# Kernel tuning notes

Hardware: AMD Instinct MI355X
Metric: run time of the kernel (lower is better)

## Reference

```python
import jax, jax.numpy as jnp
import numpy as np

BLOCK = 32
# MXFP4 grid: exp_bits=2, man_bits=1, exp_bias=1 -> {0, 0.5, 1, 1.5, 2, 3, 4, 6}
GRID = jnp.array([0.0, 0.5, 1.0, 1.5, 2.0, 3.0, 4.0, 6.0], dtype=jnp.float32)
GRID_MAX = 6.0
EPS = 1e-12


def _snap_to_grid(a):
    # nearest-neighbor snap; ties go to the lower grid value (matches torch ref)
    pos = jnp.searchsorted(GRID, a)              # side='left', same as torch default
    lo = jnp.clip(pos - 1, 0, GRID.shape[0] - 1)
    hi = jnp.clip(pos, 0, GRID.shape[0] - 1)
    v_lo = GRID[lo]
    v_hi = GRID[hi]
    return jnp.where(a - v_lo > v_hi - a, v_hi, v_lo)


def quant_act_mxfp4(x):
    orig_shape = x.shape
    xb = x.astype(jnp.float32).reshape(-1, BLOCK)           # [nblk, BLOCK]
    amax = jnp.clip(jnp.max(jnp.abs(xb), axis=-1, keepdims=True), EPS)
    # scale stored in FP16 (quant_act_fp hard-codes scale_dtype='FP16')
    scale = (amax / GRID_MAX).astype(jnp.float16).astype(jnp.float32)
    x_norm = xb / jnp.clip(scale, EPS)
    snapped = _snap_to_grid(jnp.abs(x_norm))
    return (jnp.sign(x_norm) * snapped * scale).reshape(orig_shape)


def setup_inputs() -> dict:
    key = jax.random.key(0)
    k1, k2, k3 = jax.random.split(key, 3)
    x = jax.random.normal(k1, (2, 4096, 4096), dtype=jnp.float32)
    W = jax.random.normal(k2, (11008, 4096), dtype=jnp.float32)
    bias = jax.random.normal(k3, (11008,), dtype=jnp.float32)
    return {"x": x, "W": W, "bias": bias}


def reference(x, W, bias):
    # 1) dynamic per-block MXFP4 activation quantization
    x_q = quant_act_mxfp4(x)                                # [B, S, H]
    # 2) dense GEMM: F.linear(x_q, W, bias)
    return jnp.einsum('bsh,oh->bso', x_q, W) + bias
```

## Files before the change

### kernel.cpp

```cpp
#include <hip/hip_runtime.h>


#define M_DIM 8192
#define K_DIM 4096
#define N_DIM 11008

typedef float floatx4 __attribute__((ext_vector_type(4)));
typedef _Float16 half8 __attribute__((ext_vector_type(8)));


__device__ inline float snap_mxfp4(float a) {
    float lo  = (a <= 0.25f) ? 0.0f : ((a <= 0.75f) ? 0.5f : 1.0f);
    float mid = (a <= 1.75f) ? 1.5f : 2.0f;
    float hi  = (a <= 3.5f)  ? 3.0f : ((a <= 5.0f) ? 4.0f : 6.0f);
    return (a <= 1.25f) ? lo : ((a <= 2.5f) ? mid : hi);
}

#define QUANT_BLOCKS 16384
#define CONV_BLOCKS  22016

__global__ __launch_bounds__(256) void prep_kernel(
        const float* __restrict__ x, _Float16* __restrict__ xq,
        const float* __restrict__ W, _Float16* __restrict__ wq) {
    if (blockIdx.x < QUANT_BLOCKS) {
        size_t t    = (size_t)blockIdx.x * 256 + threadIdx.x;
        size_t base = t * 8;
        const float4* p = (const float4*)(x + base);
        float4 v0 = p[0];
        float4 v1 = p[1];
        float in[8] = {v0.x, v0.y, v0.z, v0.w, v1.x, v1.y, v1.z, v1.w};

        float a0 = fmaxf(fmaxf(fabsf(in[0]), fabsf(in[1])), fmaxf(fabsf(in[2]), fabsf(in[3])));
        float a1 = fmaxf(fmaxf(fabsf(in[4]), fabsf(in[5])), fmaxf(fabsf(in[6]), fabsf(in[7])));
        float amax = fmaxf(a0, a1);
        amax = fmaxf(amax, __shfl_xor(amax, 1));
        amax = fmaxf(amax, __shfl_xor(amax, 2));
        amax = fmaxf(amax, 1e-12f);

        float scale = (float)(_Float16)(amax / 6.0f);
        float sdiv  = fmaxf(scale, 1e-12f);

        union { _Float16 h[8]; uint4 v; } o;
#pragma unroll
        for (int i = 0; i < 8; ++i) {
            float xn = in[i] / sdiv;
            float s  = snap_mxfp4(fabsf(xn));
            o.h[i]   = (_Float16)copysignf(s * scale, xn);
        }
        *(uint4*)(xq + base) = o.v;
    } else {
        size_t t    = (size_t)(blockIdx.x - QUANT_BLOCKS) * 256 + threadIdx.x;
        size_t base = t * 8;
        const float4* p = (const float4*)(W + base);
        float4 v0 = p[0];
        float4 v1 = p[1];
        float in[8] = {v0.x, v0.y, v0.z, v0.w, v1.x, v1.y, v1.z, v1.w};
        union { _Float16 h[8]; uint4 v; } o;
#pragma unroll
        for (int i = 0; i < 8; ++i) o.h[i] = (_Float16)in[i];
        *(uint4*)(wq + base) = o.v;
    }
}


#define BM 128
#define BN 128
#define BK 32
#define M_TILES 64
#define N_TILES 86
#define BANDW 32

__global__ __launch_bounds__(256) void gemm_f16_kernel(
        const _Float16* __restrict__ A, const _Float16* __restrict__ B,
        const float* __restrict__ bias, float* __restrict__ C) {
    __shared__ __align__(16) _Float16 sA[BM * BK];
    __shared__ __align__(16) _Float16 sB[BN * BK];

    const int tid   = threadIdx.x;
    const int lane  = tid & 63;
    const int wave  = tid >> 6;
    const int wr    = wave >> 1;
    const int wc    = wave & 1;
    const int mlane = lane & 15;
    const int kq    = lane >> 4;

    int pid = blockIdx.x;
    int mTile, nTile;
    if (pid < M_TILES * BANDW * 2) {
        int band = pid >> 11;
        int rem  = pid & 2047;
        nTile = (band << 5) + (rem & 31);
        mTile = rem >> 5;
    } else {
        int rem = pid - M_TILES * BANDW * 2;
        nTile = 64 + rem % 22;
        mTile = rem / 22;
    }
    const int rowStart = mTile * BM;
    const int colStart = nTile * BN;

    const int p0 = tid, p1 = tid + 256;
    const int r0 = p0 >> 2, r1 = p1 >> 2;
    const int kc0 = (p0 & 3) ^ (r0 & 3);
    const int kc1 = (p1 & 3) ^ (r1 & 3);
    const _Float16* aSrc0 = A + (size_t)(rowStart + r0) * K_DIM + kc0 * 8;
    const _Float16* aSrc1 = A + (size_t)(rowStart + r1) * K_DIM + kc1 * 8;
    const _Float16* bSrc0 = B + (size_t)(colStart + r0) * K_DIM + kc0 * 8;
    const _Float16* bSrc1 = B + (size_t)(colStart + r1) * K_DIM + kc1 * 8;

    _Float16* ldsA0 = sA + (wave * 64) * 8;
    _Float16* ldsA1 = sA + (256 + wave * 64) * 8;
    _Float16* ldsB0 = sB + (wave * 64) * 8;
    _Float16* ldsB1 = sB + (256 + wave * 64) * 8;

    int aOff[4], bOff[4];
#pragma unroll
    for (int i = 0; i < 4; ++i) {
        int row = wr * 64 + i * 16 + mlane;
        aOff[i] = (row * 4 + (kq ^ (row & 3))) * 8;
        int col = wc * 64 + i * 16 + mlane;
        bOff[i] = (col * 4 + (kq ^ (col & 3))) * 8;
    }

    floatx4 acc[4][4];
    const floatx4 z4 = {0.f, 0.f, 0.f, 0.f};
#pragma unroll
    for (int i = 0; i < 4; ++i)
#pragma unroll
        for (int j = 0; j < 4; ++j) acc[i][j] = z4;

#define ISSUE_LOADS(K0)                                                            \
    do {                                                                           \
        __builtin_amdgcn_global_load_lds(                                          \
            (const __attribute__((address_space(1))) unsigned int*)(const void*)(aSrc0 + (K0)), \
            (__attribute__((address_space(3))) unsigned int*)(void*)ldsA0, 16, 0, 0); \
        __builtin_amdgcn_global_load_lds(                                          \
            (const __attribute__((address_space(1))) unsigned int*)(const void*)(aSrc1 + (K0)), \
            (__attribute__((address_space(3))) unsigned int*)(void*)ldsA1, 16, 0, 0); \
        __builtin_amdgcn_global_load_lds(                                          \
            (const __attribute__((address_space(1))) unsigned int*)(const void*)(bSrc0 + (K0)), \
            (__attribute__((address_space(3))) unsigned int*)(void*)ldsB0, 16, 0, 0); \
        __builtin_amdgcn_global_load_lds(                                          \
            (const __attribute__((address_space(1))) unsigned int*)(const void*)(bSrc1 + (K0)), \
            (__attribute__((address_space(3))) unsigned int*)(void*)ldsB1, 16, 0, 0); \
    } while (0)

    ISSUE_LOADS(0);

    for (int k0 = 0; k0 < K_DIM; k0 += BK) {
        __syncthreads();

        half8 af[4], bf[4];
#pragma unroll
        for (int i = 0; i < 4; ++i) {
            af[i] = *(const half8*)(sA + aOff[i]);
            bf[i] = *(const half8*)(sB + bOff[i]);
        }

        __syncthreads();

        if (k0 + BK < K_DIM) ISSUE_LOADS(k0 + BK);

#pragma unroll
        for (int mt = 0; mt < 4; ++mt)
#pragma unroll
            for (int nt = 0; nt < 4; ++nt)
                acc[mt][nt] = __builtin_amdgcn_mfma_f32_16x16x32_f16(
                    af[mt], bf[nt], acc[mt][nt], 0, 0, 0);
    }

#pragma unroll
    for (int mt = 0; mt < 4; ++mt) {
        int gm = rowStart + wr * 64 + mt * 16 + kq * 4;
#pragma unroll
        for (int nt = 0; nt < 4; ++nt) {
            int gn = colStart + wc * 64 + nt * 16 + mlane;
            float bv = bias[gn];
#pragma unroll
            for (int r = 0; r < 4; ++r)
                C[(size_t)(gm + r) * N_DIM + gn] = acc[mt][nt][r] + bv;
        }
    }
}


extern "C" void kernel_launch(void* const* d_in, const int* in_sizes, int n_in,
                              void* d_out, int out_size, void* d_ws, size_t ws_size,
                              hipStream_t stream) {
    const float* x    = (const float*)d_in[0];
    const float* W    = (const float*)d_in[1];
    const float* bias = (const float*)d_in[2];
    float* out = (float*)d_out;

    _Float16* Aq = (_Float16*)d_ws;
    _Float16* Wq = Aq + (size_t)M_DIM * K_DIM;

    prep_kernel<<<QUANT_BLOCKS + CONV_BLOCKS, 256, 0, stream>>>(x, Aq, W, Wq);
    gemm_f16_kernel<<<M_TILES * N_TILES, 256, 0, stream>>>(Aq, Wq, bias, out);
}
```

Before: 1.477 ms.

## Rewrite GEMM as 256x256 double-buffered 8-wave kernel with phased MFMA scheduling

Replaces the 128x128 tile, BK=32 GEMM with a 256x256 tile, BK=64 kernel using 512 threads, a 128KB double-buffered LDS staging area fed by global_load_lds, and an XCD-aware block swizzle. Each K tile is split into four phases separated by explicit barriers and waitcnts, with s_setprio raised around the MFMA groups, so that global loads for the next tile overlap the math on the current one. This is meant to increase data reuse per byte loaded and hide memory latency. In exchange, register pressure is higher (32 accumulators per lane), the large LDS footprint limits occupancy, and the hand-written waitcnt scheduling is fragile.

```diff
diff --git a/kernel.cpp b/kernel.cpp
--- a/kernel.cpp
+++ b/kernel.cpp
@@ -63,122 +63,144 @@
 }
 
 
-#define BM 128
-#define BN 128
-#define BK 32
-#define M_TILES 64
-#define N_TILES 86
-#define BANDW 32
-
-__global__ __launch_bounds__(256) void gemm_f16_kernel(
+#define M_TILES 32
+#define N_TILES 43
+#define K_TILES 64
+
+#define GLDS(gp, lo) __builtin_amdgcn_global_load_lds(                        \
+    (const __attribute__((address_space(1))) unsigned int*)(const void*)(gp), \
+    (__attribute__((address_space(3))) unsigned int*)(void*)(lds + (lo)), 16, 0, 0)
+
+#define ISSUE_TILE(bo, ko) do {                        \
+    GLDS(aS + (ko),               (bo) +         stW); \
+    GLDS(aS + (ko) +  64*K_DIM,   (bo) +  8192 + stW); \
+    GLDS(bS + (ko),               (bo) + 32768 + stW); \
+    GLDS(bS + (ko) +  64*K_DIM,   (bo) + 40960 + stW); \
+    GLDS(bS + (ko) + 128*K_DIM,   (bo) + 49152 + stW); \
+    GLDS(bS + (ko) + 192*K_DIM,   (bo) + 57344 + stW); \
+    GLDS(aS + (ko) + 128*K_DIM,   (bo) + 16384 + stW); \
+    GLDS(aS + (ko) + 192*K_DIM,   (bo) + 24576 + stW); \
+  } while (0)
+
+#define LDA(bo, mh, m, cp) (*(const half8*)(lds + (bo) + (mh)*16384 + (m)*2048 + aRd + (cp)))
+#define LDB(bo, q,  cp)    (*(const half8*)(lds + (bo) + ((q)>>1)*16384 + ((q)&1)*2048 + bRd + (cp)))
+
+#define BAR()   __builtin_amdgcn_s_barrier()
+#define LGKM0() do { asm volatile("s_waitcnt lgkmcnt(0)" ::: "memory");      \
+                     __builtin_amdgcn_sched_barrier(0); } while (0)
+#define VMW(n)  asm volatile("s_waitcnt vmcnt(" #n ")" ::: "memory")
+
+#define MFMA16(rb) do {                                                                        \
+    acc[(rb)+0][0] = __builtin_amdgcn_mfma_f32_16x16x32_f16(a0, b0, acc[(rb)+0][0], 0, 0, 0);  \
+    acc[(rb)+1][0] = __builtin_amdgcn_mfma_f32_16x16x32_f16(a1, b0, acc[(rb)+1][0], 0, 0, 0);  \
+    acc[(rb)+2][0] = __builtin_amdgcn_mfma_f32_16x16x32_f16(a2, b0, acc[(rb)+2][0], 0, 0, 0);  \
+    acc[(rb)+3][0] = __builtin_amdgcn_mfma_f32_16x16x32_f16(a3, b0, acc[(rb)+3][0], 0, 0, 0);  \
+    acc[(rb)+0][1] = __builtin_amdgcn_mfma_f32_16x16x32_f16(a0, b1, acc[(rb)+0][1], 0, 0, 0);  \
+    acc[(rb)+1][1] = __builtin_amdgcn_mfma_f32_16x16x32_f16(a1, b1, acc[(rb)+1][1], 0, 0, 0);  \
+    acc[(rb)+2][1] = __builtin_amdgcn_mfma_f32_16x16x32_f16(a2, b1, acc[(rb)+2][1], 0, 0, 0);  \
+    acc[(rb)+3][1] = __builtin_amdgcn_mfma_f32_16x16x32_f16(a3, b1, acc[(rb)+3][1], 0, 0, 0);  \
+    acc[(rb)+0][2] = __builtin_amdgcn_mfma_f32_16x16x32_f16(a0, b2, acc[(rb)+0][2], 0, 0, 0);  \
+    acc[(rb)+1][2] = __builtin_amdgcn_mfma_f32_16x16x32_f16(a1, b2, acc[(rb)+1][2], 0, 0, 0);  \
+    acc[(rb)+2][2] = __builtin_amdgcn_mfma_f32_16x16x32_f16(a2, b2, acc[(rb)+2][2], 0, 0, 0);  \
+    acc[(rb)+3][2] = __builtin_amdgcn_mfma_f32_16x16x32_f16(a3, b2, acc[(rb)+3][2], 0, 0, 0);  \
+    acc[(rb)+0][3] = __builtin_amdgcn_mfma_f32_16x16x32_f16(a0, b3, acc[(rb)+0][3], 0, 0, 0);  \
+    acc[(rb)+1][3] = __builtin_amdgcn_mfma_f32_16x16x32_f16(a1, b3, acc[(rb)+1][3], 0, 0, 0);  \
+    acc[(rb)+2][3] = __builtin_amdgcn_mfma_f32_16x16x32_f16(a2, b3, acc[(rb)+2][3], 0, 0, 0);  \
+    acc[(rb)+3][3] = __builtin_amdgcn_mfma_f32_16x16x32_f16(a3, b3, acc[(rb)+3][3], 0, 0, 0);  \
+  } while (0)
+
+#define TILE(BO, ISSUE_STMT, VM1_STMT, VM4_STMT) do {                                     \
+                                           \
+    a0=LDA(BO,0,0,cp0); a1=LDA(BO,0,1,cp0); a2=LDA(BO,0,2,cp0); a3=LDA(BO,0,3,cp0);       \
+    b0=LDB(BO,0,cp0);   b1=LDB(BO,1,cp0);   b2=LDB(BO,2,cp0);   b3=LDB(BO,3,cp0);         \
+    ISSUE_STMT;                                                                           \
+    BAR(); LGKM0();                                                                       \
+    __builtin_amdgcn_s_setprio(1); MFMA16(0); __builtin_amdgcn_s_setprio(0);              \
+    VM1_STMT; BAR();                                                                      \
+                                                       \
+    a0=LDA(BO,1,0,cp0); a1=LDA(BO,1,1,cp0); a2=LDA(BO,1,2,cp0); a3=LDA(BO,1,3,cp0);       \
+    BAR(); LGKM0();                                                                       \
+    __builtin_amdgcn_s_setprio(1); MFMA16(4); __builtin_amdgcn_s_setprio(0);              \
+    BAR();                                                                                \
+                                                                        \
+    a0=LDA(BO,1,0,cp1); a1=LDA(BO,1,1,cp1); a2=LDA(BO,1,2,cp1); a3=LDA(BO,1,3,cp1);       \
+    b0=LDB(BO,0,cp1);   b1=LDB(BO,1,cp1);   b2=LDB(BO,2,cp1);   b3=LDB(BO,3,cp1);         \
+    BAR(); LGKM0();                                                                       \
+    __builtin_amdgcn_s_setprio(1); MFMA16(4); __builtin_amdgcn_s_setprio(0);              \
+    BAR();                                                                                \
+                                                       \
+    a0=LDA(BO,0,0,cp1); a1=LDA(BO,0,1,cp1); a2=LDA(BO,0,2,cp1); a3=LDA(BO,0,3,cp1);       \
+    BAR(); LGKM0();                                                                       \
+    __builtin_amdgcn_s_setprio(1); MFMA16(0); __builtin_amdgcn_s_setprio(0);              \
+    VM4_STMT; BAR();                                                                      \
+  } while (0)
+
+__global__ __launch_bounds__(512, 2) void gemm_f16_kernel(
         const _Float16* __restrict__ A, const _Float16* __restrict__ B,
         const float* __restrict__ bias, float* __restrict__ C) {
-    __shared__ __align__(16) _Float16 sA[BM * BK];
-    __shared__ __align__(16) _Float16 sB[BN * BK];
-
-    const int tid   = threadIdx.x;
-    const int lane  = tid & 63;
-    const int wave  = tid >> 6;
-    const int wr    = wave >> 1;
-    const int wc    = wave & 1;
-    const int mlane = lane & 15;
-    const int kq    = lane >> 4;
-
-    int pid = blockIdx.x;
-    int mTile, nTile;
-    if (pid < M_TILES * BANDW * 2) {
-        int band = pid >> 11;
-        int rem  = pid & 2047;
-        nTile = (band << 5) + (rem & 31);
-        mTile = rem >> 5;
-    } else {
-        int rem = pid - M_TILES * BANDW * 2;
-        nTile = 64 + rem % 22;
-        mTile = rem / 22;
+    __shared__ __align__(16) char lds[131072];
+
+    const int tid  = threadIdx.x;
+    const int lane = tid & 63;
+    const int wave = tid >> 6;
+    const int wm   = wave >> 2;
+    const int wn   = wave & 3;
+    const int l15  = lane & 15;
+    const int kq   = lane >> 4;
+
+    const int bid = blockIdx.x;
+    const int swz = (bid & 7) * 172 + (bid >> 3);
+    const int mT  = swz / N_TILES;
+    const int nT  = swz - mT * N_TILES;
+    const int rowStart = mT << 8;
+    const int colStart = nT << 8;
+
+    const int r0   = tid >> 3;
+    const int cSrc = (tid & 7) ^ (r0 & 7);
+    const _Float16* aS = A + (size_t)(rowStart + r0) * K_DIM + cSrc * 8;
+    const _Float16* bS = B + (size_t)(colStart + r0) * K_DIM + cSrc * 8;
+    const int stW = wave * 1024;
+
+    const int cp0 = ((kq)     ^ (lane & 7)) << 4;
+    const int cp1 = ((4 + kq) ^ (lane & 7)) << 4;
+    const int aRd = (wm * 64 + l15) * 128;
+    const int bRd = (wn * 32 + l15) * 128 + 32768;
+
+    floatx4 acc[8][4];
+    const floatx4 z4 = {0.f, 0.f, 0.f, 0.f};
+#pragma unroll
+    for (int i = 0; i < 8; ++i)
+#pragma unroll
+        for (int j = 0; j < 4; ++j) acc[i][j] = z4;
+
+    half8 a0, a1, a2, a3, b0, b1, b2, b3;
+
+    ISSUE_TILE(0, 0);
+    VMW(2);
+    BAR();
+
+#pragma unroll 1
+    for (int t = 0; t < K_TILES - 2; t += 2) {
+        const int ko1 = (t + 1) * 64;
+        const int ko2 = (t + 2) * 64;
+        TILE(0,     ISSUE_TILE(65536, ko1), VMW(8), VMW(2));
+        TILE(65536, ISSUE_TILE(0,     ko2), VMW(8), VMW(2));
     }
-    const int rowStart = mTile * BM;
-    const int colStart = nTile * BN;
-
-    const int p0 = tid, p1 = tid + 256;
-    const int r0 = p0 >> 2, r1 = p1 >> 2;
-    const int kc0 = (p0 & 3) ^ (r0 & 3);
-    const int kc1 = (p1 & 3) ^ (r1 & 3);
-    const _Float16* aSrc0 = A + (size_t)(rowStart + r0) * K_DIM + kc0 * 8;
-    const _Float16* aSrc1 = A + (size_t)(rowStart + r1) * K_DIM + kc1 * 8;
-    const _Float16* bSrc0 = B + (size_t)(colStart + r0) * K_DIM + kc0 * 8;
-    const _Float16* bSrc1 = B + (size_t)(colStart + r1) * K_DIM + kc1 * 8;
-
-    _Float16* ldsA0 = sA + (wave * 64) * 8;
-    _Float16* ldsA1 = sA + (256 + wave * 64) * 8;
-    _Float16* ldsB0 = sB + (wave * 64) * 8;
-    _Float16* ldsB1 = sB + (256 + wave * 64) * 8;
-
-    int aOff[4], bOff[4];
-#pragma unroll
-    for (int i = 0; i < 4; ++i) {
-        int row = wr * 64 + i * 16 + mlane;
-        aOff[i] = (row * 4 + (kq ^ (row & 3))) * 8;
-        int col = wc * 64 + i * 16 + mlane;
-        bOff[i] = (col * 4 + (kq ^ (col & 3))) * 8;
-    }
-
-    floatx4 acc[4][4];
-    const floatx4 z4 = {0.f, 0.f, 0.f, 0.f};
-#pragma unroll
-    for (int i = 0; i < 4; ++i)
-#pragma unroll
-        for (int j = 0; j < 4; ++j) acc[i][j] = z4;
-
-#define ISSUE_LOADS(K0)                                                            \
-    do {                                                                           \
-        __builtin_amdgcn_global_load_lds(                                          \
-            (const __attribute__((address_space(1))) unsigned int*)(const void*)(aSrc0 + (K0)), \
-            (__attribute__((address_space(3))) unsigned int*)(void*)ldsA0, 16, 0, 0); \
-        __builtin_amdgcn_global_load_lds(                                          \
-            (const __attribute__((address_space(1))) unsigned int*)(const void*)(aSrc1 + (K0)), \
-            (__attribute__((address_space(3))) unsigned int*)(void*)ldsA1, 16, 0, 0); \
-        __builtin_amdgcn_global_load_lds(                                          \
-            (const __attribute__((address_space(1))) unsigned int*)(const void*)(bSrc0 + (K0)), \
-            (__attribute__((address_space(3))) unsigned int*)(void*)ldsB0, 16, 0, 0); \
-        __builtin_amdgcn_global_load_lds(                                          \
-            (const __attribute__((address_space(1))) unsigned int*)(const void*)(bSrc1 + (K0)), \
-            (__attribute__((address_space(3))) unsigned int*)(void*)ldsB1, 16, 0, 0); \
-    } while (0)
-
-    ISSUE_LOADS(0);
-
-    for (int k0 = 0; k0 < K_DIM; k0 += BK) {
-        __syncthreads();
-
-        half8 af[4], bf[4];
-#pragma unroll
-        for (int i = 0; i < 4; ++i) {
-            af[i] = *(const half8*)(sA + aOff[i]);
-            bf[i] = *(const half8*)(sB + bOff[i]);
-        }
-
-        __syncthreads();
-
-        if (k0 + BK < K_DIM) ISSUE_LOADS(k0 + BK);
-
-#pragma unroll
-        for (int mt = 0; mt < 4; ++mt)
-#pragma unroll
-            for (int nt = 0; nt < 4; ++nt)
-                acc[mt][nt] = __builtin_amdgcn_mfma_f32_16x16x32_f16(
-                    af[mt], bf[nt], acc[mt][nt], 0, 0, 0);
-    }
-
-#pragma unroll
-    for (int mt = 0; mt < 4; ++mt) {
-        int gm = rowStart + wr * 64 + mt * 16 + kq * 4;
-#pragma unroll
-        for (int nt = 0; nt < 4; ++nt) {
-            int gn = colStart + wc * 64 + nt * 16 + mlane;
-            float bv = bias[gn];
-#pragma unroll
-            for (int r = 0; r < 4; ++r)
-                C[(size_t)(gm + r) * N_DIM + gn] = acc[mt][nt][r] + bv;
+    TILE(0,     ISSUE_TILE(65536, (K_TILES - 1) * 64), VMW(8), VMW(2));
+    TILE(65536, (void)0, VMW(0), (void)0);
+
+    const int cRow = kq * 4;
+#pragma unroll
+    for (int r = 0; r < 8; ++r) {
+        const int gm = rowStart + (r >> 2) * 128 + wm * 64 + (r & 3) * 16 + cRow;
+#pragma unroll
+        for (int q = 0; q < 4; ++q) {
+            const int gn = colStart + (q >> 1) * 128 + wn * 32 + (q & 1) * 16 + l15;
+            const float bv = bias[gn];
+            float* cptr = C + (size_t)gm * N_DIM + gn;
+#pragma unroll
+            for (int e = 0; e < 4; ++e)
+                cptr[(size_t)e * N_DIM] = acc[r][q][e] + bv;
         }
     }
 }
@@ -196,5 +218,5 @@
     _Float16* Wq = Aq + (size_t)M_DIM * K_DIM;
 
     prep_kernel<<<QUANT_BLOCKS + CONV_BLOCKS, 256, 0, stream>>>(x, Aq, W, Wq);
-    gemm_f16_kernel<<<M_TILES * N_TILES, 256, 0, stream>>>(Aq, Wq, bias, out);
-}
+    gemm_f16_kernel<<<M_TILES * N_TILES, 512, 0, stream>>>(Aq, Wq, bias, out);
+}
```

Measured after the change: 1.252 ms. 15.2% less time.
